# Kernel tuning notes

Measured on AMD Instinct MI355X. Metric: run time of the kernel, lower is better.

The kernel has to match this reference:

```python
import jax, jax.numpy as jnp
import numpy as np

N = 4096          # num_nodes
E = 65536         # num edges (avg degree 16)
WALK_LENGTH = 16
OUT_DIM = 8


def setup_inputs() -> dict:
    key = jax.random.key(0)
    k1, k2 = jax.random.split(key, 2)
    edge_index = jax.random.randint(k1, (2, E), 0, N, dtype=jnp.int64)
    # nn.Linear(walk_length, out_dim): weight [out_dim, walk_length], bias [out_dim]
    linear_w = (jax.random.normal(k2, (OUT_DIM, WALK_LENGTH), jnp.float32)
                / np.float32(np.sqrt(WALK_LENGTH)))
    linear_b = jnp.zeros((OUT_DIM,), jnp.float32)
    return {"edge_index": edge_index, "num_nodes": N,
            "linear_w": linear_w, "linear_b": linear_b}


def reference(edge_index, num_nodes, linear_w, linear_b):
    row, col = edge_index[0], edge_index[1]
    # out-degree via scatter_add, clamped to >= 1
    deg = jnp.zeros((num_nodes,), jnp.float32).at[row].add(1.0)
    deg = jnp.maximum(deg, 1.0)
    rw_values = 1.0 / deg[row]                              # [E]
    # random-walk transition matrix P[row, col] = 1/deg[row]
    # (.at[].add sums duplicate edges, matching coalesce())
    P = jnp.zeros((num_nodes, num_nodes), jnp.float32).at[row, col].add(rw_values)
    Pt = P.T

    def step(cur, _):
        cur = Pt @ cur                                      # [N, N]
        return cur, jnp.diagonal(cur)                       # k-step return probs

    cur0 = jnp.eye(num_nodes, dtype=jnp.float32)
    _, diags = jax.lax.scan(step, cur0, None, length=WALK_LENGTH)
    rw_diag = diags.T                                       # [N, walk_length]
    return rw_diag @ linear_w.T + linear_b                  # [N, out_dim]
```

## Files before the change

kernel.cpp:

```cpp
#include <hip/hip_runtime.h>
#include <hip/hip_fp16.h>
#include <hip/hip_fp8.h>

#define NNODES 4096
#define LWALK 16
#define ODIM 8

#define FP8_SCALE 256.0f
#define FP8_INV   0.00390625f
#define FP8_INV2  1.52587890625e-05f

typedef unsigned int uint4n __attribute__((ext_vector_type(4)));
typedef unsigned int uint2n __attribute__((ext_vector_type(2)));
typedef float float2n __attribute__((ext_vector_type(2)));

__device__ __forceinline__ void dec8f(unsigned int lo, unsigned int hi, float* f) {
#if __has_builtin(__builtin_amdgcn_cvt_pk_f32_fp8)
    float2n p;
    p = __builtin_amdgcn_cvt_pk_f32_fp8((int)lo, false); f[0] = p.x; f[1] = p.y;
    p = __builtin_amdgcn_cvt_pk_f32_fp8((int)lo, true);  f[2] = p.x; f[3] = p.y;
    p = __builtin_amdgcn_cvt_pk_f32_fp8((int)hi, false); f[4] = p.x; f[5] = p.y;
    p = __builtin_amdgcn_cvt_pk_f32_fp8((int)hi, true);  f[6] = p.x; f[7] = p.y;
#else
    unsigned int w[2] = {lo, hi};
    const unsigned char* b = (const unsigned char*)w;
#pragma unroll
    for (int i = 0; i < 8; ++i) {
        __hip_fp8_e4m3 t; t.__x = b[i]; f[i] = (float)t;
    }
#endif
}

__device__ __forceinline__ void enc8f(const float* a, unsigned int* lo,
                                      unsigned int* hi) {
#if __has_builtin(__builtin_amdgcn_cvt_pk_fp8_f32)
    int l = 0, h = 0;
    l = __builtin_amdgcn_cvt_pk_fp8_f32(a[0], a[1], l, false);
    l = __builtin_amdgcn_cvt_pk_fp8_f32(a[2], a[3], l, true);
    h = __builtin_amdgcn_cvt_pk_fp8_f32(a[4], a[5], h, false);
    h = __builtin_amdgcn_cvt_pk_fp8_f32(a[6], a[7], h, true);
    *lo = (unsigned int)l; *hi = (unsigned int)h;
#else
    unsigned char b[8];
#pragma unroll
    for (int i = 0; i < 8; ++i)
        b[i] = __hip_cvt_float_to_fp8(a[i], __HIP_SATFINITE, __HIP_E4M3);
    unsigned int w[2];
    __builtin_memcpy(w, b, 8);
    *lo = w[0]; *hi = w[1];
#endif
}

__global__ void detect_fmt_k(const void* ei, int E, int* flag) {
    if (blockIdx.x == 0 && threadIdx.x == 0) {
        const long long* p = (const long long*)ei;
        int ok = 1;
        for (int i = 0; i < 64; ++i) {
            long long v = p[i];
            if (v < 0 || v >= NNODES) { ok = 0; break; }
        }
        *flag = ok;
    }
}

__device__ __forceinline__ int load_idx(const void* p, int i, int fmt) {
    if (fmt) return (int)((const long long*)p)[i];
    return ((const int*)p)[i];
}

__global__ void build_deg_cnt_k(const void* ei, int E, int* deg, int* cnt,
                                const int* fmt) {
    int e = blockIdx.x * blockDim.x + threadIdx.x;
    if (e >= E) return;
    int f = *fmt;
    int r = load_idx(ei, e, f);
    int c = load_idx(ei, E + e, f);
    atomicAdd(&deg[r], 1);
    atomicAdd(&cnt[c], 1);
}

__global__ void scan_k(const int* __restrict__ cnt, int* __restrict__ rowptr,
                       int* __restrict__ cursor) {
    __shared__ int sm[1024];
    int tid = threadIdx.x;
    int v0 = (cnt[4 * tid + 0] + 7) & ~7;
    int v1 = (cnt[4 * tid + 1] + 7) & ~7;
    int v2 = (cnt[4 * tid + 2] + 7) & ~7;
    int v3 = (cnt[4 * tid + 3] + 7) & ~7;
    int tsum = v0 + v1 + v2 + v3;
    sm[tid] = tsum;
    __syncthreads();
    int val = tsum;
    for (int off = 1; off < 1024; off <<= 1) {
        int t = (tid >= off) ? sm[tid - off] : 0;
        __syncthreads();
        val += t;
        sm[tid] = val;
        __syncthreads();
    }
    int excl = val - tsum;
    int p0 = excl, p1 = excl + v0, p2 = p1 + v1, p3 = p2 + v2;
    rowptr[4 * tid + 0] = p0; rowptr[4 * tid + 1] = p1;
    rowptr[4 * tid + 2] = p2; rowptr[4 * tid + 3] = p3;
    cursor[4 * tid + 0] = p0; cursor[4 * tid + 1] = p1;
    cursor[4 * tid + 2] = p2; cursor[4 * tid + 3] = p3;
    if (tid == 1023) rowptr[4096] = val;
}

__global__ void fill_csr_k(const void* ei, int E, const int* __restrict__ deg,
                           int* cursor, uint2* __restrict__ epad, const int* fmt) {
    int e = blockIdx.x * blockDim.x + threadIdx.x;
    if (e >= E) return;
    int f = *fmt;
    int r = load_idx(ei, e, f);
    int c = load_idx(ei, E + e, f);
    int pos = atomicAdd(&cursor[c], 1);
    int d = deg[r];
    float v = 1.0f / (float)(d < 1 ? 1 : d);
    epad[pos] = make_uint2((unsigned)r, __float_as_uint(v));
}

__global__ void pad_fill_k(const int* __restrict__ rowptr,
                           const int* __restrict__ cursor,
                           uint2* __restrict__ epad) {
    int c = blockIdx.x * blockDim.x + threadIdx.x;
    if (c >= NNODES) return;
    for (int p = cursor[c]; p < rowptr[c + 1]; ++p)
        epad[p] = make_uint2(0u, 0u);
}

__global__ void zero_k(uint4n* p) {
    int i = blockIdx.x * blockDim.x + threadIdx.x;
    uint4n z = {0u, 0u, 0u, 0u};
    p[i] = z;
}

__global__ void x1scatter_k(const void* ei, int E, const int* __restrict__ deg,
                            __half* __restrict__ X1, const int* fmt) {
    int e = blockIdx.x * blockDim.x + threadIdx.x;
    if (e >= E) return;
    int f = *fmt;
    int r = load_idx(ei, e, f);
    int c = load_idx(ei, E + e, f);
    int d = deg[r];
    float v = 1.0f / (float)(d < 1 ? 1 : d);
    size_t idx = (size_t)c * NNODES + r;
    unsigned int* base = (unsigned int*)(X1 + (idx & ~(size_t)1));
    bool hi = (idx & 1) != 0;
    unsigned int old = *base, assumed;
    do {
        assumed = old;
        unsigned short cur = hi ? (unsigned short)(assumed >> 16)
                                : (unsigned short)(assumed & 0xFFFFu);
        float nf = __half2float(__ushort_as_half(cur)) + v;
        unsigned short ns = __half_as_ushort(__float2half(nf));
        unsigned int nv = hi ? ((assumed & 0x0000FFFFu) | ((unsigned int)ns << 16))
                             : ((assumed & 0xFFFF0000u) | ns);
        old = atomicCAS(base, assumed, nv);
    } while (old != assumed);
}

__global__ void diag1_k(const __half* __restrict__ X1, float* __restrict__ rw) {
    int i = blockIdx.x * blockDim.x + threadIdx.x;
    if (i < NNODES)
        rw[i * LWALK + 0] = __half2float(X1[(size_t)i * NNODES + i]);
}

__global__ __launch_bounds__(256) void spmm_hh_k(
    const __half* __restrict__ X, __half* __restrict__ Y,
    const int* __restrict__ rowptr, const uint2* __restrict__ epad,
    float* __restrict__ rw, int kcol) {
    const int bid = blockIdx.x;
    const int slab = bid & 7;
    const int lane = threadIdx.x & 63;
    const int c =
        __builtin_amdgcn_readfirstlane((bid >> 3) * 4 + (threadIdx.x >> 6));
    const int colo = slab * 512 + lane * 8;
    const __half* Xs = X + colo;
    const int beg = rowptr[c], end = rowptr[c + 1];
    float a[8];
#pragma unroll
    for (int u = 0; u < 8; ++u) a[u] = 0.f;
    for (int e = beg; e < end; e += 8) {
        uint2 ed[8];
#pragma unroll
        for (int j = 0; j < 8; ++j) ed[j] = epad[e + j];
        uint4n x[8];
#pragma unroll
        for (int j = 0; j < 8; ++j)
            x[j] = *(const uint4n*)(Xs + (size_t)ed[j].x * NNODES);
#pragma unroll
        for (int j = 0; j < 8; ++j) {
            float v = __uint_as_float(ed[j].y);
            const __half* h = (const __half*)&x[j];
#pragma unroll
            for (int u = 0; u < 8; ++u)
                a[u] = fmaf(__half2float(h[u]), v, a[u]);
        }
    }
    if ((c >> 9) == slab && lane == ((c & 511) >> 3)) {
        float d = 0.f;
#pragma unroll
        for (int u = 0; u < 8; ++u)
            if ((c & 7) == u) d = a[u];
        rw[c * LWALK + kcol] = d;
    }
    uint4n o;
    __half2 oh[4];
#pragma unroll
    for (int u = 0; u < 4; ++u) oh[u] = __floats2half2_rn(a[2 * u], a[2 * u + 1]);
    o.x = *(unsigned int*)&oh[0];
    o.y = *(unsigned int*)&oh[1];
    o.z = *(unsigned int*)&oh[2];
    o.w = *(unsigned int*)&oh[3];
    __builtin_nontemporal_store(o, (uint4n*)(Y + (size_t)c * NNODES + colo));
}

__global__ __launch_bounds__(256) void spmm_h8_k(
    const __half* __restrict__ X, unsigned char* __restrict__ Y8,
    const int* __restrict__ rowptr, const uint2* __restrict__ epad,
    float* __restrict__ rw, int kcol) {
    const int bid = blockIdx.x;
    const int slab = bid & 7;
    const int lane = threadIdx.x & 63;
    const int c =
        __builtin_amdgcn_readfirstlane((bid >> 3) * 4 + (threadIdx.x >> 6));
    const int colo = slab * 512 + lane * 8;
    const __half* Xs = X + colo;
    const int beg = rowptr[c], end = rowptr[c + 1];
    float a[8];
#pragma unroll
    for (int u = 0; u < 8; ++u) a[u] = 0.f;
    for (int e = beg; e < end; e += 8) {
        uint2 ed[8];
#pragma unroll
        for (int j = 0; j < 8; ++j) ed[j] = epad[e + j];
        uint4n x[8];
#pragma unroll
        for (int j = 0; j < 8; ++j)
            x[j] = *(const uint4n*)(Xs + (size_t)ed[j].x * NNODES);
#pragma unroll
        for (int j = 0; j < 8; ++j) {
            float v = __uint_as_float(ed[j].y);
            const __half* h = (const __half*)&x[j];
#pragma unroll
            for (int u = 0; u < 8; ++u)
                a[u] = fmaf(__half2float(h[u]), v, a[u]);
        }
    }
    if ((c >> 9) == slab && lane == ((c & 511) >> 3)) {
        float d = 0.f;
#pragma unroll
        for (int u = 0; u < 8; ++u)
            if ((c & 7) == u) d = a[u];
        rw[c * LWALK + kcol] = d;
    }
    float s[8];
#pragma unroll
    for (int u = 0; u < 8; ++u) s[u] = a[u] * FP8_SCALE;
    unsigned int lo, hi;
    enc8f(s, &lo, &hi);
    uint2n o;
    o.x = lo; o.y = hi;
    __builtin_nontemporal_store(o, (uint2n*)(Y8 + (size_t)c * NNODES + colo));
}

__global__ __launch_bounds__(256) void spmm_88_k(
    const unsigned char* __restrict__ X8, unsigned char* __restrict__ Y8,
    const int* __restrict__ rowptr, const uint2* __restrict__ epad,
    float* __restrict__ rw, int kcol) {
    const int bid = blockIdx.x;
    const int slab = bid & 7;
    const int lane = threadIdx.x & 63;
    const int c =
        __builtin_amdgcn_readfirstlane((bid >> 3) * 4 + (threadIdx.x >> 6));
    const int colo = slab * 512 + lane * 8;
    const unsigned char* Xs = X8 + colo;
    const int beg = rowptr[c], end = rowptr[c + 1];
    float a[8];
#pragma unroll
    for (int u = 0; u < 8; ++u) a[u] = 0.f;
    for (int e = beg; e < end; e += 8) {
        uint2 ed[8];
#pragma unroll
        for (int j = 0; j < 8; ++j) ed[j] = epad[e + j];
        uint2n x[8];
#pragma unroll
        for (int j = 0; j < 8; ++j)
            x[j] = *(const uint2n*)(Xs + (size_t)ed[j].x * NNODES);
#pragma unroll
        for (int j = 0; j < 8; ++j) {
            float v = __uint_as_float(ed[j].y);
            float f[8];
            dec8f(x[j].x, x[j].y, f);
#pragma unroll
            for (int u = 0; u < 8; ++u) a[u] = fmaf(f[u], v, a[u]);
        }
    }
    if ((c >> 9) == slab && lane == ((c & 511) >> 3)) {
        float d = 0.f;
#pragma unroll
        for (int u = 0; u < 8; ++u)
            if ((c & 7) == u) d = a[u];
        rw[c * LWALK + kcol] = d * FP8_INV;
    }
    unsigned int lo, hi;
    enc8f(a, &lo, &hi);
    uint2n o;
    o.x = lo; o.y = hi;
    __builtin_nontemporal_store(o, (uint2n*)(Y8 + (size_t)c * NNODES + colo));
}

__global__ __launch_bounds__(256) void pairdiag8_k(
    const unsigned char* __restrict__ A, const unsigned char* __restrict__ B,
    float* __restrict__ rw, int col_odd, int col_even) {
    __shared__ float bt[64][65];
    __shared__ float ct[64][65];
    const int i0 = blockIdx.x * 64;
    const int t = threadIdx.x;
    const int li = t >> 2;
    const int q = t & 3;
    const int c0 = q * 16;
    const int Jbeg = blockIdx.y * (NNODES / 16);
    const int Jend = Jbeg + (NNODES / 16);
    float accO = 0.f, accE = 0.f;
    for (int J = Jbeg; J < Jend; J += 64) {
        uint4n b16 = *(const uint4n*)(B + (size_t)(J + li) * NNODES + i0 + c0);
        uint4n g16 = *(const uint4n*)(A + (size_t)(J + li) * NNODES + i0 + c0);
        __syncthreads();
        float bf[16], gf[16];
        dec8f(b16.x, b16.y, bf);
        dec8f(b16.z, b16.w, bf + 8);
        dec8f(g16.x, g16.y, gf);
        dec8f(g16.z, g16.w, gf + 8);
#pragma unroll
        for (int s = 0; s < 16; ++s) {
            bt[c0 + s][li] = bf[s];
            ct[c0 + s][li] = gf[s];
        }
        __syncthreads();
        uint4n a16 = *(const uint4n*)(A + (size_t)(i0 + li) * NNODES + J + c0);
        float af[16];
        dec8f(a16.x, a16.y, af);
        dec8f(a16.z, a16.w, af + 8);
#pragma unroll
        for (int s = 0; s < 16; ++s) {
            accO = fmaf(af[s], bt[li][c0 + s], accO);
            accE = fmaf(af[s], ct[li][c0 + s], accE);
        }
    }
    accO += __shfl_xor(accO, 1);
    accO += __shfl_xor(accO, 2);
    accE += __shfl_xor(accE, 1);
    accE += __shfl_xor(accE, 2);
    if (q == 0) {
        atomicAdd(&rw[(i0 + li) * LWALK + col_odd], accO * FP8_INV2);
        atomicAdd(&rw[(i0 + li) * LWALK + col_even], accE * FP8_INV2);
    }
}

__global__ void linear_k(const float* __restrict__ rw, const float* __restrict__ W,
                         const float* __restrict__ b, float* __restrict__ out) {
    int i = blockIdx.x * blockDim.x + threadIdx.x;
    if (i >= NNODES * ODIM) return;
    int s = i >> 3, d = i & 7;
    float acc = b[d];
#pragma unroll
    for (int k = 0; k < LWALK; ++k)
        acc = fmaf(rw[s * LWALK + k], W[d * LWALK + k], acc);
    out[i] = acc;
}

extern "C" void kernel_launch(void* const* d_in, const int* in_sizes, int n_in,
                              void* d_out, int out_size, void* d_ws, size_t ws_size,
                              hipStream_t stream) {
    const void* ei = d_in[0];
    int E = in_sizes[0] / 2;
    const float* W = (const float*)d_in[2];
    const float* bias = (const float*)d_in[3];
    float* out = (float*)d_out;

    char* ws = (char*)d_ws;
    size_t off = 0;
    auto alloc = [&](size_t bytes) -> char* {
        char* p = ws + off;
        off = (off + bytes + 255) & ~(size_t)255;
        return p;
    };
    int* flag = (int*)alloc(4);
    int* deg = (int*)alloc(NNODES * 4);
    int* cnt = (int*)alloc(NNODES * 4);
    int* rowptr = (int*)alloc((NNODES + 1) * 4);
    int* cursor = (int*)alloc(NNODES * 4);
    uint2* epad = (uint2*)alloc(((size_t)E + 8 * NNODES) * 8);
    float* rw = (float*)alloc(NNODES * LWALK * 4);
    __half* Xh = (__half*)alloc((size_t)NNODES * NNODES * 2);
    __half* Yh = (__half*)alloc((size_t)NNODES * NNODES * 2);
    unsigned char* F0 = (unsigned char*)alloc((size_t)NNODES * NNODES);
    unsigned char* F1 = (unsigned char*)alloc((size_t)NNODES * NNODES);

    (void)hipMemsetAsync(deg, 0, NNODES * 4, stream);
    (void)hipMemsetAsync(cnt, 0, NNODES * 4, stream);
    (void)hipMemsetAsync(rw, 0, NNODES * LWALK * 4, stream);
    detect_fmt_k<<<1, 64, 0, stream>>>(ei, E, flag);
    build_deg_cnt_k<<<(E + 255) / 256, 256, 0, stream>>>(ei, E, deg, cnt, flag);
    scan_k<<<1, 1024, 0, stream>>>(cnt, rowptr, cursor);
    fill_csr_k<<<(E + 255) / 256, 256, 0, stream>>>(ei, E, deg, cursor, epad, flag);
    pad_fill_k<<<(NNODES + 255) / 256, 256, 0, stream>>>(rowptr, cursor, epad);

    zero_k<<<NNODES * (NNODES / 8) / 256, 256, 0, stream>>>((uint4n*)Xh);
    x1scatter_k<<<(E + 255) / 256, 256, 0, stream>>>(ei, E, deg, Xh, flag);
    diag1_k<<<(NNODES + 255) / 256, 256, 0, stream>>>(Xh, rw);

    const int SG = NNODES * 8 / 4;
    dim3 pg(NNODES / 64, 16);

    spmm_hh_k<<<SG, 256, 0, stream>>>(Xh, Yh, rowptr, epad, rw, 1);
    spmm_h8_k<<<SG, 256, 0, stream>>>(Yh, F0, rowptr, epad, rw, 2);
    spmm_88_k<<<SG, 256, 0, stream>>>(F0, F1, rowptr, epad, rw, 3);
    spmm_88_k<<<SG, 256, 0, stream>>>(F1, F0, rowptr, epad, rw, 4);
    pairdiag8_k<<<pg, 256, 0, stream>>>(F0, F1, rw, 8, 9);
    spmm_88_k<<<SG, 256, 0, stream>>>(F0, F1, rowptr, epad, rw, 5);
    pairdiag8_k<<<pg, 256, 0, stream>>>(F1, F0, rw, 10, 11);
    spmm_88_k<<<SG, 256, 0, stream>>>(F1, F0, rowptr, epad, rw, 6);
    pairdiag8_k<<<pg, 256, 0, stream>>>(F0, F1, rw, 12, 13);
    spmm_88_k<<<SG, 256, 0, stream>>>(F0, F1, rowptr, epad, rw, 7);
    pairdiag8_k<<<pg, 256, 0, stream>>>(F1, F0, rw, 14, 15);

    linear_k<<<(NNODES * ODIM + 255) / 256, 256, 0, stream>>>(rw, W, bias, out);
}
```

Measured before the change: 352.9 us.

## Fuse SpMM steps with pair-diagonal blocks and drop the fp16 intermediate

The first fp16 SpMM and the separate diag1 kernel are removed. Step 1's diagonal is now written inside spmm_h8_k, which reads the fp16 X1 and emits fp8 directly. Later fp8 SpMM steps go into one fused kernel whose grid also contains pair-diagonal blocks, so independent work shares a single launch, with a third fp8 buffer to avoid read/write conflicts. Each fp8 SpMM thread now handles 16 columns with 16-byte loads, and the pair-diagonal shared tiles use fp16 to halve LDS usage. The risks are lower occupancy from more registers per thread, mixed block types within one grid, and extra rounding in the fp16 shared tiles.

Measured after the change: 322.7 us. 1.09x faster.

```diff
diff --git a/kernel.cpp b/kernel.cpp
--- a/kernel.cpp
+++ b/kernel.cpp
@@ -49,6 +49,19 @@
     __builtin_memcpy(w, b, 8);
     *lo = w[0]; *hi = w[1];
 #endif
+}
+
+__device__ __forceinline__ void dec16f(uint4n w, float* f) {
+    dec8f(w.x, w.y, f);
+    dec8f(w.z, w.w, f + 8);
+}
+
+__device__ __forceinline__ uint4n enc16f(const float* a) {
+    uint4n o;
+    unsigned int lo, hi;
+    enc8f(a, &lo, &hi);     o.x = lo; o.y = hi;
+    enc8f(a + 8, &lo, &hi); o.z = lo; o.w = hi;
+    return o;
 }
 
 __global__ void detect_fmt_k(const void* ei, int E, int* flag) {
@@ -160,16 +173,10 @@
     } while (old != assumed);
 }
 
-__global__ void diag1_k(const __half* __restrict__ X1, float* __restrict__ rw) {
-    int i = blockIdx.x * blockDim.x + threadIdx.x;
-    if (i < NNODES)
-        rw[i * LWALK + 0] = __half2float(X1[(size_t)i * NNODES + i]);
-}
-
-__global__ __launch_bounds__(256) void spmm_hh_k(
-    const __half* __restrict__ X, __half* __restrict__ Y,
+__global__ __launch_bounds__(256) void spmm_h8_k(
+    const __half* __restrict__ X, unsigned char* __restrict__ Y8,
     const int* __restrict__ rowptr, const uint2* __restrict__ epad,
-    float* __restrict__ rw, int kcol) {
+    float* __restrict__ rw) {
     const int bid = blockIdx.x;
     const int slab = bid & 7;
     const int lane = threadIdx.x & 63;
@@ -199,61 +206,12 @@
         }
     }
     if ((c >> 9) == slab && lane == ((c & 511) >> 3)) {
+        rw[c * LWALK + 0] = __half2float(X[(size_t)c * NNODES + c]);
         float d = 0.f;
 #pragma unroll
         for (int u = 0; u < 8; ++u)
             if ((c & 7) == u) d = a[u];
-        rw[c * LWALK + kcol] = d;
-    }
-    uint4n o;
-    __half2 oh[4];
-#pragma unroll
-    for (int u = 0; u < 4; ++u) oh[u] = __floats2half2_rn(a[2 * u], a[2 * u + 1]);
-    o.x = *(unsigned int*)&oh[0];
-    o.y = *(unsigned int*)&oh[1];
-    o.z = *(unsigned int*)&oh[2];
-    o.w = *(unsigned int*)&oh[3];
-    __builtin_nontemporal_store(o, (uint4n*)(Y + (size_t)c * NNODES + colo));
-}
-
-__global__ __launch_bounds__(256) void spmm_h8_k(
-    const __half* __restrict__ X, unsigned char* __restrict__ Y8,
-    const int* __restrict__ rowptr, const uint2* __restrict__ epad,
-    float* __restrict__ rw, int kcol) {
-    const int bid = blockIdx.x;
-    const int slab = bid & 7;
-    const int lane = threadIdx.x & 63;
-    const int c =
-        __builtin_amdgcn_readfirstlane((bid >> 3) * 4 + (threadIdx.x >> 6));
-    const int colo = slab * 512 + lane * 8;
-    const __half* Xs = X + colo;
-    const int beg = rowptr[c], end = rowptr[c + 1];
-    float a[8];
-#pragma unroll
-    for (int u = 0; u < 8; ++u) a[u] = 0.f;
-    for (int e = beg; e < end; e += 8) {
-        uint2 ed[8];
-#pragma unroll
-        for (int j = 0; j < 8; ++j) ed[j] = epad[e + j];
-        uint4n x[8];
-#pragma unroll
-        for (int j = 0; j < 8; ++j)
-            x[j] = *(const uint4n*)(Xs + (size_t)ed[j].x * NNODES);
-#pragma unroll
-        for (int j = 0; j < 8; ++j) {
-            float v = __uint_as_float(ed[j].y);
-            const __half* h = (const __half*)&x[j];
-#pragma unroll
-            for (int u = 0; u < 8; ++u)
-                a[u] = fmaf(__half2float(h[u]), v, a[u]);
-        }
-    }
-    if ((c >> 9) == slab && lane == ((c & 511) >> 3)) {
-        float d = 0.f;
-#pragma unroll
-        for (int u = 0; u < 8; ++u)
-            if ((c & 7) == u) d = a[u];
-        rw[c * LWALK + kcol] = d;
+        rw[c * LWALK + 1] = d;
     }
     float s[8];
 #pragma unroll
@@ -265,97 +223,95 @@
     __builtin_nontemporal_store(o, (uint2n*)(Y8 + (size_t)c * NNODES + colo));
 }
 
-__global__ __launch_bounds__(256) void spmm_88_k(
+__global__ __launch_bounds__(256) void fused8_k(
     const unsigned char* __restrict__ X8, unsigned char* __restrict__ Y8,
     const int* __restrict__ rowptr, const uint2* __restrict__ epad,
-    float* __restrict__ rw, int kcol) {
+    float* __restrict__ rw, int kcol,
+    const unsigned char* __restrict__ PA, const unsigned char* __restrict__ PB,
+    int colO, int colE, int nspmm) {
+    __shared__ __half bt[64][66];
+    __shared__ __half ct[64][66];
     const int bid = blockIdx.x;
-    const int slab = bid & 7;
-    const int lane = threadIdx.x & 63;
-    const int c =
-        __builtin_amdgcn_readfirstlane((bid >> 3) * 4 + (threadIdx.x >> 6));
-    const int colo = slab * 512 + lane * 8;
-    const unsigned char* Xs = X8 + colo;
-    const int beg = rowptr[c], end = rowptr[c + 1];
-    float a[8];
-#pragma unroll
-    for (int u = 0; u < 8; ++u) a[u] = 0.f;
-    for (int e = beg; e < end; e += 8) {
-        uint2 ed[8];
-#pragma unroll
-        for (int j = 0; j < 8; ++j) ed[j] = epad[e + j];
-        uint2n x[8];
-#pragma unroll
-        for (int j = 0; j < 8; ++j)
-            x[j] = *(const uint2n*)(Xs + (size_t)ed[j].x * NNODES);
-#pragma unroll
-        for (int j = 0; j < 8; ++j) {
-            float v = __uint_as_float(ed[j].y);
-            float f[8];
-            dec8f(x[j].x, x[j].y, f);
-#pragma unroll
-            for (int u = 0; u < 8; ++u) a[u] = fmaf(f[u], v, a[u]);
-        }
-    }
-    if ((c >> 9) == slab && lane == ((c & 511) >> 3)) {
-        float d = 0.f;
-#pragma unroll
-        for (int u = 0; u < 8; ++u)
-            if ((c & 7) == u) d = a[u];
-        rw[c * LWALK + kcol] = d * FP8_INV;
-    }
-    unsigned int lo, hi;
-    enc8f(a, &lo, &hi);
-    uint2n o;
-    o.x = lo; o.y = hi;
-    __builtin_nontemporal_store(o, (uint2n*)(Y8 + (size_t)c * NNODES + colo));
-}
-
-__global__ __launch_bounds__(256) void pairdiag8_k(
-    const unsigned char* __restrict__ A, const unsigned char* __restrict__ B,
-    float* __restrict__ rw, int col_odd, int col_even) {
-    __shared__ float bt[64][65];
-    __shared__ float ct[64][65];
-    const int i0 = blockIdx.x * 64;
-    const int t = threadIdx.x;
-    const int li = t >> 2;
-    const int q = t & 3;
-    const int c0 = q * 16;
-    const int Jbeg = blockIdx.y * (NNODES / 16);
-    const int Jend = Jbeg + (NNODES / 16);
-    float accO = 0.f, accE = 0.f;
-    for (int J = Jbeg; J < Jend; J += 64) {
-        uint4n b16 = *(const uint4n*)(B + (size_t)(J + li) * NNODES + i0 + c0);
-        uint4n g16 = *(const uint4n*)(A + (size_t)(J + li) * NNODES + i0 + c0);
-        __syncthreads();
-        float bf[16], gf[16];
-        dec8f(b16.x, b16.y, bf);
-        dec8f(b16.z, b16.w, bf + 8);
-        dec8f(g16.x, g16.y, gf);
-        dec8f(g16.z, g16.w, gf + 8);
-#pragma unroll
-        for (int s = 0; s < 16; ++s) {
-            bt[c0 + s][li] = bf[s];
-            ct[c0 + s][li] = gf[s];
-        }
-        __syncthreads();
-        uint4n a16 = *(const uint4n*)(A + (size_t)(i0 + li) * NNODES + J + c0);
-        float af[16];
-        dec8f(a16.x, a16.y, af);
-        dec8f(a16.z, a16.w, af + 8);
-#pragma unroll
-        for (int s = 0; s < 16; ++s) {
-            accO = fmaf(af[s], bt[li][c0 + s], accO);
-            accE = fmaf(af[s], ct[li][c0 + s], accE);
-        }
-    }
-    accO += __shfl_xor(accO, 1);
-    accO += __shfl_xor(accO, 2);
-    accE += __shfl_xor(accE, 1);
-    accE += __shfl_xor(accE, 2);
-    if (q == 0) {
-        atomicAdd(&rw[(i0 + li) * LWALK + col_odd], accO * FP8_INV2);
-        atomicAdd(&rw[(i0 + li) * LWALK + col_even], accE * FP8_INV2);
+    if (bid < nspmm) {
+        const int slab = bid & 3;
+        const int lane = threadIdx.x & 63;
+        const int c =
+            __builtin_amdgcn_readfirstlane((bid >> 2) * 4 + (threadIdx.x >> 6));
+        const int colo = slab * 1024 + lane * 16;
+        const unsigned char* Xs = X8 + colo;
+        const int beg = rowptr[c], end = rowptr[c + 1];
+        float a[16];
+#pragma unroll
+        for (int u = 0; u < 16; ++u) a[u] = 0.f;
+        for (int e = beg; e < end; e += 8) {
+            uint2 ed[8];
+#pragma unroll
+            for (int j = 0; j < 8; ++j) ed[j] = epad[e + j];
+            uint4n x[8];
+#pragma unroll
+            for (int j = 0; j < 8; ++j)
+                x[j] = *(const uint4n*)(Xs + (size_t)ed[j].x * NNODES);
+#pragma unroll
+            for (int j = 0; j < 8; ++j) {
+                float v = __uint_as_float(ed[j].y);
+                float f[16];
+                dec16f(x[j], f);
+#pragma unroll
+                for (int u = 0; u < 16; ++u) a[u] = fmaf(f[u], v, a[u]);
+            }
+        }
+        if ((c >> 10) == slab && lane == ((c & 1023) >> 4)) {
+            float d = 0.f;
+#pragma unroll
+            for (int u = 0; u < 16; ++u)
+                if ((c & 15) == u) d = a[u];
+            rw[c * LWALK + kcol] = d * FP8_INV;
+        }
+        uint4n o = enc16f(a);
+        __builtin_nontemporal_store(o, (uint4n*)(Y8 + (size_t)c * NNODES + colo));
+    } else {
+        const int pb = bid - nspmm;
+        const int i0 = (pb & 63) * 64;
+        const int Jbeg = (pb >> 6) * (NNODES / 16);
+        const int Jend = Jbeg + (NNODES / 16);
+        const int t = threadIdx.x;
+        const int li = t >> 2;
+        const int q = t & 3;
+        const int c0 = q * 16;
+        float accO = 0.f, accE = 0.f;
+        for (int J = Jbeg; J < Jend; J += 64) {
+            uint4n b16 = __builtin_nontemporal_load(
+                (const uint4n*)(PB + (size_t)(J + li) * NNODES + i0 + c0));
+            uint4n g16 = __builtin_nontemporal_load(
+                (const uint4n*)(PA + (size_t)(J + li) * NNODES + i0 + c0));
+            __syncthreads();
+            float bf[16], gf[16];
+            dec16f(b16, bf);
+            dec16f(g16, gf);
+#pragma unroll
+            for (int s = 0; s < 16; ++s) {
+                bt[c0 + s][li] = __float2half(bf[s]);
+                ct[c0 + s][li] = __float2half(gf[s]);
+            }
+            __syncthreads();
+            uint4n a16 = __builtin_nontemporal_load(
+                (const uint4n*)(PA + (size_t)(i0 + li) * NNODES + J + c0));
+            float af[16];
+            dec16f(a16, af);
+#pragma unroll
+            for (int s = 0; s < 16; ++s) {
+                accO = fmaf(af[s], __half2float(bt[li][c0 + s]), accO);
+                accE = fmaf(af[s], __half2float(ct[li][c0 + s]), accE);
+            }
+        }
+        accO += __shfl_xor(accO, 1);
+        accO += __shfl_xor(accO, 2);
+        accE += __shfl_xor(accE, 1);
+        accE += __shfl_xor(accE, 2);
+        if (q == 0) {
+            atomicAdd(&rw[(i0 + li) * LWALK + colO], accO * FP8_INV2);
+            atomicAdd(&rw[(i0 + li) * LWALK + colE], accE * FP8_INV2);
+        }
     }
 }
 
@@ -395,9 +351,9 @@
     uint2* epad = (uint2*)alloc(((size_t)E + 8 * NNODES) * 8);
     float* rw = (float*)alloc(NNODES * LWALK * 4);
     __half* Xh = (__half*)alloc((size_t)NNODES * NNODES * 2);
-    __half* Yh = (__half*)alloc((size_t)NNODES * NNODES * 2);
-    unsigned char* F0 = (unsigned char*)alloc((size_t)NNODES * NNODES);
-    unsigned char* F1 = (unsigned char*)alloc((size_t)NNODES * NNODES);
+    unsigned char* A = (unsigned char*)alloc((size_t)NNODES * NNODES);
+    unsigned char* B = (unsigned char*)alloc((size_t)NNODES * NNODES);
+    unsigned char* C = (unsigned char*)alloc((size_t)NNODES * NNODES);
 
     (void)hipMemsetAsync(deg, 0, NNODES * 4, stream);
     (void)hipMemsetAsync(cnt, 0, NNODES * 4, stream);
@@ -410,22 +366,17 @@
 
     zero_k<<<NNODES * (NNODES / 8) / 256, 256, 0, stream>>>((uint4n*)Xh);
     x1scatter_k<<<(E + 255) / 256, 256, 0, stream>>>(ei, E, deg, Xh, flag);
-    diag1_k<<<(NNODES + 255) / 256, 256, 0, stream>>>(Xh, rw);
-
-    const int SG = NNODES * 8 / 4;
-    dim3 pg(NNODES / 64, 16);
-
-    spmm_hh_k<<<SG, 256, 0, stream>>>(Xh, Yh, rowptr, epad, rw, 1);
-    spmm_h8_k<<<SG, 256, 0, stream>>>(Yh, F0, rowptr, epad, rw, 2);
-    spmm_88_k<<<SG, 256, 0, stream>>>(F0, F1, rowptr, epad, rw, 3);
-    spmm_88_k<<<SG, 256, 0, stream>>>(F1, F0, rowptr, epad, rw, 4);
-    pairdiag8_k<<<pg, 256, 0, stream>>>(F0, F1, rw, 8, 9);
-    spmm_88_k<<<SG, 256, 0, stream>>>(F0, F1, rowptr, epad, rw, 5);
-    pairdiag8_k<<<pg, 256, 0, stream>>>(F1, F0, rw, 10, 11);
-    spmm_88_k<<<SG, 256, 0, stream>>>(F1, F0, rowptr, epad, rw, 6);
-    pairdiag8_k<<<pg, 256, 0, stream>>>(F0, F1, rw, 12, 13);
-    spmm_88_k<<<SG, 256, 0, stream>>>(F0, F1, rowptr, epad, rw, 7);
-    pairdiag8_k<<<pg, 256, 0, stream>>>(F1, F0, rw, 14, 15);
+
+    spmm_h8_k<<<NNODES * 8 / 4, 256, 0, stream>>>(Xh, A, rowptr, epad, rw);
+
+    const int SG = 4096;
+    fused8_k<<<SG, 256, 0, stream>>>(A, B, rowptr, epad, rw, 2, nullptr, nullptr, 0, 0, SG);
+    fused8_k<<<SG, 256, 0, stream>>>(B, C, rowptr, epad, rw, 3, nullptr, nullptr, 0, 0, SG);
+    fused8_k<<<SG, 256, 0, stream>>>(C, A, rowptr, epad, rw, 4, nullptr, nullptr, 0, 0, SG);
+    fused8_k<<<SG + 1024, 256, 0, stream>>>(A, B, rowptr, epad, rw, 5, A, C, 8, 9, SG);
+    fused8_k<<<SG + 1024, 256, 0, stream>>>(B, C, rowptr, epad, rw, 6, B, A, 10, 11, SG);
+    fused8_k<<<SG + 1024, 256, 0, stream>>>(C, A, rowptr, epad, rw, 7, C, B, 12, 13, SG);
+    fused8_k<<<1024, 256, 0, stream>>>(nullptr, nullptr, rowptr, epad, rw, 0, A, C, 14, 15, 0);
 
     linear_k<<<(NNODES * ODIM + 255) / 256, 256, 0, stream>>>(rw, W, bias, out);
 }
```
